# Optimization experiments

Measured on AMD Instinct MI355X. Metric: run time of the kernel, lower is better.

Reference implementation:

```python
import jax, jax.numpy as jnp
import numpy as np

N_HEADS = 12

def setup_inputs() -> dict:
    key = jax.random.key(0)
    k1, k2, k3 = jax.random.split(key, 3)
    B, L, D = 2, 2048, 768
    x = jax.random.normal(k1, (B, L, D), dtype=jnp.float32)
    attention_mask = jnp.ones((B, L), dtype=jnp.int32)  # 1 = real token
    w_qkv = jax.random.normal(k2, (D, 3 * D), dtype=jnp.float32) * (1.0 / np.sqrt(D))
    b_qkv = jnp.zeros((3 * D,), dtype=jnp.float32)
    w_out = jax.random.normal(k3, (D, D), dtype=jnp.float32) * (1.0 / np.sqrt(D))
    b_out = jnp.zeros((D,), dtype=jnp.float32)
    return {"x": x, "attention_mask": attention_mask, "w_qkv": w_qkv,
            "b_qkv": b_qkv, "w_out": w_out, "b_out": b_out}

def reference(x, attention_mask, w_qkv, b_qkv, w_out, b_out):
    B, L, D = x.shape
    H = N_HEADS
    dk = D // H
    # fused QKV projection
    qkv = jnp.einsum('bld,de->ble', x, w_qkv) + b_qkv  # (B,L,3D)
    q, k, v = jnp.split(qkv, 3, axis=-1)
    def to_heads(t):
        return t.reshape(B, L, H, dk).transpose(0, 2, 1, 3)  # (B,H,L,dk)
    q, k, v = to_heads(q), to_heads(k), to_heads(v)
    scale = 1.0 / jnp.sqrt(jnp.asarray(dk, dtype=x.dtype))
    scores = jnp.einsum('bhqd,bhkd->bhqk', q, k) * scale  # (B,H,L,L)
    mask = (attention_mask != 0)[:, None, None, :]  # (B,1,1,L), True = keep
    neg = jnp.asarray(jnp.finfo(scores.dtype).min, dtype=scores.dtype)
    scores = jnp.where(mask, scores, neg)
    weights = jax.nn.softmax(scores, axis=-1)
    out = jnp.einsum('bhqk,bhkd->bhqd', weights, v)  # (B,H,L,dk)
    out = out.transpose(0, 2, 1, 3).reshape(B, L, D)
    return jnp.einsum('bld,de->ble', out, w_out) + b_out
```

## Files before the change

### kernel.cpp

```cpp
#include <hip/hip_runtime.h>

typedef __bf16 bf16;
typedef bf16 bf16x4 __attribute__((ext_vector_type(4)));
typedef bf16 bf16x8 __attribute__((ext_vector_type(8)));
typedef float f32x4 __attribute__((ext_vector_type(4)));

#define MFMA16(A, B, C) __builtin_amdgcn_mfma_f32_16x16x32_bf16(A, B, C, 0, 0, 0)
#define NEG_BIG -30000.0f

#define GLOAD_LDS16(gptr, lptr)                                                \
    __builtin_amdgcn_global_load_lds(                                          \
        (__attribute__((address_space(1))) void*)(gptr),                       \
        (__attribute__((address_space(3))) void*)(lptr), 16, 0, 0)

#define SW(r, c8) ((r) * 64 + (((((c8) >> 3) ^ ((r) & 7))) << 3))
#define SW32(r, q) ((r) * 32 + ((((q) ^ ((r) & 3))) << 3))

__global__ void mark_k(float* __restrict__ out, float val, int n) {
    int i = blockIdx.x * 256 + threadIdx.x;
    if (i < n) out[i] = val;
}

__global__ __launch_bounds__(256) void cvt_x_k(const float* __restrict__ src,
                                               bf16* __restrict__ dst, int n) {
    int i = (blockIdx.x * 256 + threadIdx.x) * 8;
    if (i >= n) return;
    float4 a = *(const float4*)&src[i];
    float4 b = *(const float4*)&src[i + 4];
    bf16x8 w;
    w[0] = (bf16)a.x; w[1] = (bf16)a.y; w[2] = (bf16)a.z; w[3] = (bf16)a.w;
    w[4] = (bf16)b.x; w[5] = (bf16)b.y; w[6] = (bf16)b.z; w[7] = (bf16)b.w;
    *(bf16x8*)&dst[i] = w;
}

__global__ __launch_bounds__(256) void transpose_cvt_tiled(
    const float* __restrict__ src, bf16* __restrict__ dst, int R, int C) {
    __shared__ float t[32][33];
    int tid = threadIdx.x, tx = tid & 31, ty = tid >> 5;
    int bx = blockIdx.x * 32, by = blockIdx.y * 32;
#pragma unroll
    for (int i = 0; i < 4; ++i) {
        int row = by + ty + i * 8;
        t[ty + i * 8][tx] = src[(size_t)row * C + bx + tx];
    }
    __syncthreads();
#pragma unroll
    for (int i = 0; i < 4; ++i) {
        int outrow = bx + ty + i * 8;
        dst[(size_t)outrow * R + by + tx] = (bf16)t[tx][ty + i * 8];
    }
}

#define CLD 136

__global__ __launch_bounds__(256) void gemm_qkv_v5(
    const bf16* __restrict__ A, const bf16* __restrict__ B,
    const float* __restrict__ bias, bf16* __restrict__ Qh,
    bf16* __restrict__ Kh, bf16* __restrict__ Vth) {
    __shared__ __align__(16) bf16 SMEM[128 * CLD];
    int tid = threadIdx.x, lane = tid & 63, wave = tid >> 6;
    int quad = lane >> 4, l16 = lane & 15;
    int wr = wave >> 1, wc = wave & 1;
    int m0 = blockIdx.y * 128, n0 = blockIdx.x * 128;
    const int K = 768;
    const f32x4 fz = {0.f, 0.f, 0.f, 0.f};
    f32x4 acc[4][4];
#pragma unroll
    for (int nj = 0; nj < 4; ++nj)
#pragma unroll
        for (int mi = 0; mi < 4; ++mi) acc[nj][mi] = fz;
    const bf16* Ablk = A + (size_t)m0 * K;
    const bf16* Bblk = B + (size_t)n0 * K;
    int srow = lane >> 2, c = lane & 3;

#pragma unroll
    for (int i = 0; i < 2; ++i) {
        int r0 = i * 64 + wave * 16;
        int row = r0 + srow;
        int sc = (c ^ (row & 3)) << 3;
        GLOAD_LDS16(&Ablk[(size_t)row * K + sc], &SMEM[r0 * 32]);
        GLOAD_LDS16(&Bblk[(size_t)row * K + sc], &SMEM[4096 + r0 * 32]);
    }

    int p = 0;
    for (int k0 = 0; k0 < K; k0 += 32) {
        __syncthreads();
        if (k0 + 32 < K) {
            int kn = k0 + 32;
#pragma unroll
            for (int i = 0; i < 2; ++i) {
                int r0 = i * 64 + wave * 16;
                int row = r0 + srow;
                int sc = (c ^ (row & 3)) << 3;
                GLOAD_LDS16(&Ablk[(size_t)row * K + kn + sc],
                            &SMEM[(1 - p) * 8192 + r0 * 32]);
                GLOAD_LDS16(&Bblk[(size_t)row * K + kn + sc],
                            &SMEM[4096 + (1 - p) * 8192 + r0 * 32]);
            }
        }
        const bf16* Asp = &SMEM[p * 8192];
        const bf16* Bsp = &SMEM[4096 + p * 8192];
        bf16x8 af[4], bfv[4];
#pragma unroll
        for (int t = 0; t < 4; ++t) {
            af[t]  = *(const bf16x8*)&Asp[SW32(wr * 64 + t * 16 + l16, quad)];
            bfv[t] = *(const bf16x8*)&Bsp[SW32(wc * 64 + t * 16 + l16, quad)];
        }
#pragma unroll
        for (int nj = 0; nj < 4; ++nj)
#pragma unroll
            for (int mi = 0; mi < 4; ++mi)
                acc[nj][mi] = MFMA16(bfv[nj], af[mi], acc[nj][mi]);
        p ^= 1;
    }

    int which = n0 / 768;
    int h0 = (n0 % 768) >> 6;
    int b = m0 >> 11, l0 = m0 & 2047;
    __syncthreads();

    if (which == 2) {
#pragma unroll
        for (int nj = 0; nj < 4; ++nj) {
            int cl0 = wc * 64 + nj * 16 + quad * 4;
            float4 bv4 = *(const float4*)&bias[n0 + cl0];
            float bv[4] = {bv4.x, bv4.y, bv4.z, bv4.w};
#pragma unroll
            for (int mi = 0; mi < 4; ++mi) {
                int xrl = wr * 64 + mi * 16 + l16;
#pragma unroll
                for (int r = 0; r < 4; ++r)
                    SMEM[(cl0 + r) * CLD + xrl] = (bf16)(acc[nj][mi][r] + bv[r]);
            }
        }
    } else {
        float s = (which == 0) ? 0.18033688f : 1.0f;
#pragma unroll
        for (int nj = 0; nj < 4; ++nj) {
            int cl0 = wc * 64 + nj * 16 + quad * 4;
            float4 bv4 = *(const float4*)&bias[n0 + cl0];
            float bv[4] = {bv4.x, bv4.y, bv4.z, bv4.w};
#pragma unroll
            for (int mi = 0; mi < 4; ++mi) {
                int xrl = wr * 64 + mi * 16 + l16;
                bf16x4 v;
#pragma unroll
                for (int r = 0; r < 4; ++r) v[r] = (bf16)((acc[nj][mi][r] + bv[r]) * s);
                *(bf16x4*)&SMEM[xrl * CLD + cl0] = v;
            }
        }
    }
    __syncthreads();

    if (which == 2) {
#pragma unroll
        for (int i = 0; i < 8; ++i) {
            int idx = i * 256 + tid;
            int cl = idx >> 4, ch = idx & 15;
            int d = cl & 63, h = h0 + (cl >> 6);
            bf16x8 v = *(const bf16x8*)&SMEM[cl * CLD + ch * 8];
            *(bf16x8*)&Vth[((size_t)(b * 12 + h) * 64 + d) * 2048 + l0 + ch * 8] = v;
        }
    } else {
        bf16* dst = (which == 0) ? Qh : Kh;
#pragma unroll
        for (int i = 0; i < 8; ++i) {
            int idx = i * 256 + tid;
            int rr = idx >> 4, ch = idx & 15;
            int h = h0 + (ch >> 3), d0 = (ch & 7) * 8;
            bf16x8 v = *(const bf16x8*)&SMEM[rr * CLD + ch * 8];
            *(bf16x8*)&dst[((size_t)(b * 12 + h) * 2048 + l0 + rr) * 64 + d0] = v;
        }
    }
}

__global__ __launch_bounds__(128) void gemm_out_v4(
    const bf16* __restrict__ A, const bf16* __restrict__ B,
    const float* __restrict__ bias, float* __restrict__ C) {
    __shared__ __align__(16) bf16 As[2][128 * 32];
    __shared__ __align__(16) bf16 Bs[2][64 * 32];
    int tid = threadIdx.x, lane = tid & 63, wave = tid >> 6;
    int quad = lane >> 4, l16 = lane & 15;
    int m0 = blockIdx.y * 128, n0 = blockIdx.x * 64;
    const int K = 768, N = 768;
    const f32x4 fz = {0.f, 0.f, 0.f, 0.f};
    f32x4 acc[4][4];
#pragma unroll
    for (int mi = 0; mi < 4; ++mi)
#pragma unroll
        for (int nj = 0; nj < 4; ++nj) acc[mi][nj] = fz;
    const bf16* Ablk = A + (size_t)m0 * K;
    const bf16* Bblk = B + (size_t)n0 * K;
    int srow = lane >> 2, c = lane & 3;

#pragma unroll
    for (int i = 0; i < 4; ++i) {
        int r0 = i * 32 + wave * 16;
        int row = r0 + srow;
        int sc = (c ^ (row & 3)) << 3;
        GLOAD_LDS16(&Ablk[(size_t)row * K + sc], &As[0][r0 * 32]);
    }
#pragma unroll
    for (int i = 0; i < 2; ++i) {
        int r0 = i * 32 + wave * 16;
        int row = r0 + srow;
        int sc = (c ^ (row & 3)) << 3;
        GLOAD_LDS16(&Bblk[(size_t)row * K + sc], &Bs[0][r0 * 32]);
    }

    int p = 0;
    for (int k0 = 0; k0 < K; k0 += 32) {
        __syncthreads();
        if (k0 + 32 < K) {
            int kn = k0 + 32;
#pragma unroll
            for (int i = 0; i < 4; ++i) {
                int r0 = i * 32 + wave * 16;
                int row = r0 + srow;
                int sc = (c ^ (row & 3)) << 3;
                GLOAD_LDS16(&Ablk[(size_t)row * K + kn + sc], &As[1 - p][r0 * 32]);
            }
#pragma unroll
            for (int i = 0; i < 2; ++i) {
                int r0 = i * 32 + wave * 16;
                int row = r0 + srow;
                int sc = (c ^ (row & 3)) << 3;
                GLOAD_LDS16(&Bblk[(size_t)row * K + kn + sc], &Bs[1 - p][r0 * 32]);
            }
        }
        bf16x8 af[4], bfv[4];
#pragma unroll
        for (int t = 0; t < 4; ++t) {
            af[t]  = *(const bf16x8*)&As[p][SW32(wave * 64 + t * 16 + l16, quad)];
            bfv[t] = *(const bf16x8*)&Bs[p][SW32(t * 16 + l16, quad)];
        }
#pragma unroll
        for (int mi = 0; mi < 4; ++mi)
#pragma unroll
            for (int nj = 0; nj < 4; ++nj)
                acc[mi][nj] = MFMA16(af[mi], bfv[nj], acc[mi][nj]);
        p ^= 1;
    }

#pragma unroll
    for (int nj = 0; nj < 4; ++nj) {
        int col = n0 + nj * 16 + l16;
        float bv = bias[col];
#pragma unroll
        for (int mi = 0; mi < 4; ++mi)
#pragma unroll
            for (int r = 0; r < 4; ++r) {
                int row = m0 + wave * 64 + mi * 16 + quad * 4 + r;
                C[(size_t)row * N + col] = acc[mi][nj][r] + bv;
            }
    }
}

__global__ __launch_bounds__(256) void flash_attn(
    const bf16* __restrict__ Q, const bf16* __restrict__ K,
    const bf16* __restrict__ V, const int* __restrict__ mask,
    bf16* __restrict__ po0, bf16* __restrict__ po1, float* __restrict__ lbuf) {
    __shared__ __align__(16) bf16 Ks[2][64 * 64];
    __shared__ __align__(16) bf16 Vs[2][64 * 64];
    __shared__ float maskS[1024];
    __shared__ int cleanF;

    int tid = threadIdx.x, lane = tid & 63, wave = tid >> 6;
    int quad = lane >> 4, l16 = lane & 15;

    int n = blockIdx.x;
    int xcd = n & 7, idx = n >> 3;
    int g = xcd * 6 + (idx >> 4);
    int m = idx & 15;
    int bh = g % 24;
    int split = g / 24;
    int b = bh / 12;
    int s0 = split * 1024;
    int q0 = m * 128 + wave * 32;

    bf16x8 aq[2][2];
#pragma unroll
    for (int qt = 0; qt < 2; ++qt) {
        const bf16* Qp = Q + ((size_t)bh * 2048 + q0 + qt * 16 + l16) * 64;
        aq[qt][0] = *(const bf16x8*)(Qp + quad * 8);
        aq[qt][1] = *(const bf16x8*)(Qp + 32 + quad * 8);
    }

    if (tid == 0) cleanF = 1;
    __syncthreads();
    const int* mrow = mask + b * 2048 + s0;
    int myclean = 1;
#pragma unroll
    for (int i = 0; i < 4; ++i) {
        int idx2 = i * 256 + tid;
        int mv = mrow[idx2];
        maskS[idx2] = mv ? 0.0f : NEG_BIG;
        myclean &= (mv != 0);
    }
    if (!myclean) cleanF = 0;

    const f32x4 fz = {0.f, 0.f, 0.f, 0.f};
    f32x4 o[2][4];
    float l_i[2] = {0.f, 0.f};
#pragma unroll
    for (int qt = 0; qt < 2; ++qt)
#pragma unroll
        for (int dt = 0; dt < 4; ++dt) o[qt][dt] = fz;

    int srow = tid >> 3;
    int sc8  = (tid & 7) * 8;
    const bf16* Kbase = K + ((size_t)bh * 2048 + s0) * 64;
    const bf16* Vbase = V + (size_t)bh * 64 * 2048 + s0;

#pragma unroll
    for (int i = 0; i < 2; ++i) {
        int row = srow + i * 32;
        *(bf16x8*)&Ks[0][SW(row, sc8)] =
            *(const bf16x8*)&Kbase[(size_t)row * 64 + sc8];
        *(bf16x8*)&Vs[0][SW(row, sc8)] =
            *(const bf16x8*)&Vbase[(size_t)row * 2048 + sc8];
    }
    __syncthreads();
    int clean = cleanF;

    int p = 0;
    for (int kb = 0; kb < 1024; kb += 64) {
        bf16x8 kreg[2], vreg[2];
        const int pref = (kb + 64 < 1024);
        if (pref) {
            int nb = kb + 64;
#pragma unroll
            for (int i = 0; i < 2; ++i) {
                int row = srow + i * 32;
                kreg[i] = *(const bf16x8*)&Kbase[(size_t)(nb + row) * 64 + sc8];
                vreg[i] = *(const bf16x8*)&Vbase[(size_t)row * 2048 + nb + sc8];
            }
        }

        f32x4 s[2][4];
#pragma unroll
        for (int ct = 0; ct < 4; ++ct) {
            int krow = ct * 16 + l16;
            bf16x8 kf0 = *(const bf16x8*)&Ks[p][SW(krow, quad * 8)];
            bf16x8 kf1 = *(const bf16x8*)&Ks[p][SW(krow, 32 + quad * 8)];
#pragma unroll
            for (int qt = 0; qt < 2; ++qt) {
                f32x4 t = fz;
                t = MFMA16(kf0, aq[qt][0], t);
                t = MFMA16(kf1, aq[qt][1], t);
                s[qt][ct] = t;
            }
        }

        if (!clean) {
#pragma unroll
            for (int ct = 0; ct < 4; ++ct) {
                float4 mv = *(const float4*)&maskS[kb + ct * 16 + quad * 4];
                float ma[4] = {mv.x, mv.y, mv.z, mv.w};
#pragma unroll
                for (int qt = 0; qt < 2; ++qt)
#pragma unroll
                    for (int r = 0; r < 4; ++r) s[qt][ct][r] += ma[r];
            }
        }

        bf16x8 vf[2][4];
#pragma unroll
        for (int ks = 0; ks < 2; ++ks)
#pragma unroll
            for (int dt = 0; dt < 4; ++dt)
                vf[ks][dt] = *(const bf16x8*)&Vs[p][SW(dt * 16 + l16, ks * 32 + quad * 8)];

#pragma unroll
        for (int qt = 0; qt < 2; ++qt) {
#pragma unroll
            for (int ct = 0; ct < 4; ++ct)
#pragma unroll
                for (int r = 0; r < 4; ++r)
                    s[qt][ct][r] = __builtin_amdgcn_exp2f(s[qt][ct][r]);
            float t0 = (s[qt][0][0] + s[qt][0][1]) + (s[qt][0][2] + s[qt][0][3]);
            float t1 = (s[qt][1][0] + s[qt][1][1]) + (s[qt][1][2] + s[qt][1][3]);
            float t2 = (s[qt][2][0] + s[qt][2][1]) + (s[qt][2][2] + s[qt][2][3]);
            float t3 = (s[qt][3][0] + s[qt][3][1]) + (s[qt][3][2] + s[qt][3][3]);
            l_i[qt] += (t0 + t1) + (t2 + t3);

            unsigned pk0[4], pk1[4];
#pragma unroll
            for (int ct = 0; ct < 4; ++ct) {
                asm("v_cvt_pk_bf16_f32 %0, %1, %2"
                    : "=v"(pk0[ct]) : "v"(s[qt][ct][0]), "v"(s[qt][ct][1]));
                asm("v_cvt_pk_bf16_f32 %0, %1, %2"
                    : "=v"(pk1[ct]) : "v"(s[qt][ct][2]), "v"(s[qt][ct][3]));
            }

#pragma unroll
            for (int ks = 0; ks < 2; ++ks) {
                unsigned a0 = pk0[2 * ks], c0 = pk0[2 * ks + 1];
                unsigned b0 = pk1[2 * ks], d0 = pk1[2 * ks + 1];
                asm("v_permlane32_swap_b32 %0, %1" : "+v"(a0), "+v"(c0));
                asm("v_permlane16_swap_b32 %0, %1" : "+v"(a0), "+v"(c0));
                asm("v_permlane32_swap_b32 %0, %1" : "+v"(b0), "+v"(d0));
                asm("v_permlane16_swap_b32 %0, %1" : "+v"(b0), "+v"(d0));
                union { unsigned u[4]; bf16x8 v; } ap;
                ap.u[0] = a0;
                ap.u[1] = b0;
                ap.u[2] = c0;
                ap.u[3] = d0;
#pragma unroll
                for (int dt = 0; dt < 4; ++dt)
                    o[qt][dt] = MFMA16(ap.v, vf[ks][dt], o[qt][dt]);
            }
        }

        if (pref) {
#pragma unroll
            for (int i = 0; i < 2; ++i) {
                int row = srow + i * 32;
                *(bf16x8*)&Ks[1 - p][SW(row, sc8)] = kreg[i];
                *(bf16x8*)&Vs[1 - p][SW(row, sc8)] = vreg[i];
            }
        }
        __syncthreads();
        p ^= 1;
    }

    int h = bh % 12;
    bf16* obase = split ? po1 : po0;
#pragma unroll
    for (int qt = 0; qt < 2; ++qt) {
        l_i[qt] += __shfl_xor(l_i[qt], 16);
        l_i[qt] += __shfl_xor(l_i[qt], 32);
#pragma unroll
        for (int dt = 0; dt < 4; ++dt)
#pragma unroll
            for (int r = 0; r < 4; ++r) {
                int qrow = q0 + qt * 16 + quad * 4 + r;
                obase[((size_t)b * 2048 + qrow) * 768 + h * 64 + dt * 16 + l16] =
                    (bf16)o[qt][dt][r];
            }
        if (quad == 0) {
            int qrow = q0 + qt * 16 + l16;
            lbuf[((size_t)split * 24 + bh) * 2048 + qrow] = l_i[qt];
        }
    }
}

__global__ __launch_bounds__(256) void merge_k(
    bf16* __restrict__ ctx, const bf16* __restrict__ po1,
    const float* __restrict__ lbuf) {
    int idx = blockIdx.x * 256 + threadIdx.x;
    if (idx >= 4096 * 768 / 8) return;
    size_t i8 = (size_t)idx * 8;
    int row = (int)(i8 / 768);
    int col = (int)(i8 % 768);
    int bh = (row >> 11) * 12 + (col >> 6);
    int qrow = row & 2047;
    float l0 = lbuf[(size_t)bh * 2048 + qrow];
    float l1 = lbuf[(size_t)(24 + bh) * 2048 + qrow];
    float inv = 1.0f / (l0 + l1);
    bf16x8 v0 = *(const bf16x8*)&ctx[i8];
    bf16x8 v1 = *(const bf16x8*)&po1[i8];
    bf16x8 o;
#pragma unroll
    for (int k = 0; k < 8; ++k)
        o[k] = (bf16)(((float)v0[k] + (float)v1[k]) * inv);
    *(bf16x8*)&ctx[i8] = o;
}

extern "C" void kernel_launch(void* const* d_in, const int* in_sizes, int n_in,
                              void* d_out, int out_size, void* d_ws, size_t ws_size,
                              hipStream_t stream) {
    float* out = (float*)d_out;

    const float* x = nullptr; const int* mask = nullptr;
    const float* w_qkv = nullptr; const float* b_qkv = nullptr;
    const float* w_out = nullptr; const float* b_out = nullptr;
    int found = 0;
    for (int i = 0; i < n_in; ++i) {
        switch (in_sizes[i]) {
            case 3145728: x     = (const float*)d_in[i]; found |= 1;  break;
            case 4096:    mask  = (const int*)  d_in[i]; found |= 2;  break;
            case 1769472: w_qkv = (const float*)d_in[i]; found |= 4;  break;
            case 2304:    b_qkv = (const float*)d_in[i]; found |= 8;  break;
            case 589824:  w_out = (const float*)d_in[i]; found |= 16; break;
            case 768:     b_out = (const float*)d_in[i]; found |= 32; break;
        }
    }
    if (found != 63) {
        mark_k<<<(out_size + 255) / 256, 256, 0, stream>>>(
            out, 200.0f + (float)found, out_size);
        return;
    }

    const int M = 4096, D = 768, N3 = 2304;
    const size_t HEADS_ELEMS = (size_t)24 * 2048 * 64;

    bf16* ws    = (bf16*)d_ws;
    bf16* Kh    = ws;
    bf16* Vth   = Kh + HEADS_ELEMS;
    bf16* ctx   = Vth + HEADS_ELEMS;
    bf16* wqkvT = ctx + (size_t)M * D;
    bf16* woutT = wqkvT + (size_t)N3 * D;
    bf16* Qh    = (bf16*)d_out;
    bf16* xb    = (bf16*)d_out + HEADS_ELEMS;
    bf16* po1   = xb;
    float* lbuf = (float*)wqkvT;

    cvt_x_k<<<(M * D / 8 + 255) / 256, 256, 0, stream>>>(x, xb, M * D);
    transpose_cvt_tiled<<<dim3(2304 / 32, 768 / 32), 256, 0, stream>>>(
        w_qkv, wqkvT, 768, 2304);
    transpose_cvt_tiled<<<dim3(768 / 32, 768 / 32), 256, 0, stream>>>(
        w_out, woutT, 768, 768);

    gemm_qkv_v5<<<dim3(N3 / 128, M / 128), 256, 0, stream>>>(
        xb, wqkvT, b_qkv, Qh, Kh, Vth);

    flash_attn<<<dim3(768), 256, 0, stream>>>(
        Qh, Kh, Vth, mask, ctx, po1, lbuf);

    merge_k<<<(4096 * 768 / 8 + 255) / 256, 256, 0, stream>>>(ctx, po1, lbuf);

    gemm_out_v4<<<dim3(D / 64, M / 128), 128, 0, stream>>>(
        ctx, woutT, b_out, out);
}
```

Before: 174.3 us.

## Split attention KV range four ways when workspace allows, raise MFMA priority

Flash attention now splits the key range into four chunks instead of two when the workspace is large enough. This doubles the block count to 1536 and shortens each block's loop, and the merge kernel sums four partial outputs and denominators. It also raises wave priority around the MFMA section with s_setprio. In exchange the merge kernel moves more data, and the mask loop is no longer unrolled because its trip count is now a runtime value.

```diff
diff --git a/kernel.cpp b/kernel.cpp
--- a/kernel.cpp
+++ b/kernel.cpp
@@ -259,7 +259,8 @@
 __global__ __launch_bounds__(256) void flash_attn(
     const bf16* __restrict__ Q, const bf16* __restrict__ K,
     const bf16* __restrict__ V, const int* __restrict__ mask,
-    bf16* __restrict__ po0, bf16* __restrict__ po1, float* __restrict__ lbuf) {
+    bf16* __restrict__ po0, bf16* __restrict__ po1, bf16* __restrict__ po2,
+    bf16* __restrict__ po3, float* __restrict__ lbuf, int splits, int sblk) {
     __shared__ __align__(16) bf16 Ks[2][64 * 64];
     __shared__ __align__(16) bf16 Vs[2][64 * 64];
     __shared__ float maskS[1024];
@@ -270,12 +271,12 @@
 
     int n = blockIdx.x;
     int xcd = n & 7, idx = n >> 3;
-    int g = xcd * 6 + (idx >> 4);
+    int g = xcd * 3 * splits + (idx >> 4);
     int m = idx & 15;
     int bh = g % 24;
     int split = g / 24;
     int b = bh / 12;
-    int s0 = split * 1024;
+    int s0 = split * sblk;
     int q0 = m * 128 + wave * 32;
 
     bf16x8 aq[2][2];
@@ -290,8 +291,7 @@
     __syncthreads();
     const int* mrow = mask + b * 2048 + s0;
     int myclean = 1;
-#pragma unroll
-    for (int i = 0; i < 4; ++i) {
+    for (int i = 0; i < (sblk >> 8); ++i) {
         int idx2 = i * 256 + tid;
         int mv = mrow[idx2];
         maskS[idx2] = mv ? 0.0f : NEG_BIG;
@@ -324,9 +324,9 @@
     int clean = cleanF;
 
     int p = 0;
-    for (int kb = 0; kb < 1024; kb += 64) {
+    for (int kb = 0; kb < sblk; kb += 64) {
         bf16x8 kreg[2], vreg[2];
-        const int pref = (kb + 64 < 1024);
+        const int pref = (kb + 64 < sblk);
         if (pref) {
             int nb = kb + 64;
 #pragma unroll
@@ -337,6 +337,7 @@
             }
         }
 
+        __builtin_amdgcn_s_setprio(1);
         f32x4 s[2][4];
 #pragma unroll
         for (int ct = 0; ct < 4; ++ct) {
@@ -411,6 +412,7 @@
                     o[qt][dt] = MFMA16(ap.v, vf[ks][dt], o[qt][dt]);
             }
         }
+        __builtin_amdgcn_s_setprio(0);
 
         if (pref) {
 #pragma unroll
@@ -425,7 +427,7 @@
     }
 
     int h = bh % 12;
-    bf16* obase = split ? po1 : po0;
+    bf16* obase = (split == 0) ? po0 : (split == 1) ? po1 : (split == 2) ? po2 : po3;
 #pragma unroll
     for (int qt = 0; qt < 2; ++qt) {
         l_i[qt] += __shfl_xor(l_i[qt], 16);
@@ -447,7 +449,8 @@
 
 __global__ __launch_bounds__(256) void merge_k(
     bf16* __restrict__ ctx, const bf16* __restrict__ po1,
-    const float* __restrict__ lbuf) {
+    const bf16* __restrict__ po2, const bf16* __restrict__ po3,
+    const float* __restrict__ lbuf, int splits) {
     int idx = blockIdx.x * 256 + threadIdx.x;
     if (idx >= 4096 * 768 / 8) return;
     size_t i8 = (size_t)idx * 8;
@@ -455,15 +458,26 @@
     int col = (int)(i8 % 768);
     int bh = (row >> 11) * 12 + (col >> 6);
     int qrow = row & 2047;
-    float l0 = lbuf[(size_t)bh * 2048 + qrow];
-    float l1 = lbuf[(size_t)(24 + bh) * 2048 + qrow];
-    float inv = 1.0f / (l0 + l1);
+    float l = lbuf[(size_t)bh * 2048 + qrow] +
+              lbuf[(size_t)(24 + bh) * 2048 + qrow];
+    if (splits == 4)
+        l += lbuf[(size_t)(48 + bh) * 2048 + qrow] +
+             lbuf[(size_t)(72 + bh) * 2048 + qrow];
+    float inv = 1.0f / l;
     bf16x8 v0 = *(const bf16x8*)&ctx[i8];
     bf16x8 v1 = *(const bf16x8*)&po1[i8];
+    float acc[8];
+#pragma unroll
+    for (int k = 0; k < 8; ++k) acc[k] = (float)v0[k] + (float)v1[k];
+    if (splits == 4) {
+        bf16x8 v2 = *(const bf16x8*)&po2[i8];
+        bf16x8 v3 = *(const bf16x8*)&po3[i8];
+#pragma unroll
+        for (int k = 0; k < 8; ++k) acc[k] += (float)v2[k] + (float)v3[k];
+    }
     bf16x8 o;
 #pragma unroll
-    for (int k = 0; k < 8; ++k)
-        o[k] = (bf16)(((float)v0[k] + (float)v1[k]) * inv);
+    for (int k = 0; k < 8; ++k) o[k] = (bf16)(acc[k] * inv);
     *(bf16x8*)&ctx[i8] = o;
 }
 
@@ -506,6 +520,14 @@
     bf16* po1   = xb;
     float* lbuf = (float*)wqkvT;
 
+    bf16* po2_c = woutT + (size_t)D * D;
+    bf16* po3_c = po2_c + (size_t)M * D;
+    size_t need4 = (size_t)(po3_c + (size_t)M * D - ws) * sizeof(bf16);
+    int splits = (ws_size >= need4) ? 4 : 2;
+    int sblk = 2048 / splits;
+    bf16* po2 = (splits == 4) ? po2_c : po1;
+    bf16* po3 = (splits == 4) ? po3_c : po1;
+
     cvt_x_k<<<(M * D / 8 + 255) / 256, 256, 0, stream>>>(x, xb, M * D);
     transpose_cvt_tiled<<<dim3(2304 / 32, 768 / 32), 256, 0, stream>>>(
         w_qkv, wqkvT, 768, 2304);
@@ -515,10 +537,11 @@
     gemm_qkv_v5<<<dim3(N3 / 128, M / 128), 256, 0, stream>>>(
         xb, wqkvT, b_qkv, Qh, Kh, Vth);
 
-    flash_attn<<<dim3(768), 256, 0, stream>>>(
-        Qh, Kh, Vth, mask, ctx, po1, lbuf);
-
-    merge_k<<<(4096 * 768 / 8 + 255) / 256, 256, 0, stream>>>(ctx, po1, lbuf);
+    flash_attn<<<dim3(384 * splits), 256, 0, stream>>>(
+        Qh, Kh, Vth, mask, ctx, po1, po2, po3, lbuf, splits, sblk);
+
+    merge_k<<<(4096 * 768 / 8 + 255) / 256, 256, 0, stream>>>(
+        ctx, po1, po2, po3, lbuf, splits);
 
     gemm_out_v4<<<dim3(D / 64, M / 128), 128, 0, stream>>>(
         ctx, woutT, b_out, out);
```

Measured after the change: 185.3 us. 1.06x slower.
